# Kernel tuning notes

Hardware: AMD Instinct MI355X
Metric: run time of the kernel (lower is better)

Reference implementation:

```python
import jax, jax.numpy as jnp
import numpy as np

N_NODES = 100000
N_EDGES = 1600000
N_GRAPHS = 1024
D_NODE = 128
D_EDGE = 32
H1 = 64
H2 = 16


def _p(key, shape):
    return jax.random.normal(key, shape, dtype=jnp.float32) * 0.05


def setup_inputs() -> dict:
    key = jax.random.key(0)
    ks = jax.random.split(key, 24)
    x = jax.random.normal(ks[0], (N_NODES, D_NODE), dtype=jnp.float32)
    edge_index = jax.random.randint(ks[1], (2, N_EDGES), 0, N_NODES, dtype=jnp.int64)
    edge_attr = jax.random.normal(ks[2], (N_EDGES, D_EDGE), dtype=jnp.float32)
    batch = jnp.sort(jax.random.randint(ks[3], (N_NODES,), 0, N_GRAPHS, dtype=jnp.int64))
    # layer 1 (TransformerConv in=128, out=64, edge_dim=32, heads=1)
    Wq1, bq1 = _p(ks[4], (D_NODE, H1)), _p(ks[5], (H1,))
    Wk1, bk1 = _p(ks[6], (D_NODE, H1)), _p(ks[7], (H1,))
    Wv1, bv1 = _p(ks[8], (D_NODE, H1)), _p(ks[9], (H1,))
    We1 = _p(ks[10], (D_EDGE, H1))  # lin_edge has no bias in PyG
    Ws1, bs1 = _p(ks[11], (D_NODE, H1)), _p(ks[12], (H1,))  # skip / root weight
    # layer 2 (in=64, out=16)
    Wq2, bq2 = _p(ks[13], (H1, H2)), _p(ks[14], (H2,))
    Wk2, bk2 = _p(ks[15], (H1, H2)), _p(ks[16], (H2,))
    Wv2, bv2 = _p(ks[17], (H1, H2)), _p(ks[18], (H2,))
    We2 = _p(ks[19], (D_EDGE, H2))
    Ws2, bs2 = _p(ks[20], (H1, H2)), _p(ks[21], (H2,))
    # final fc
    Wf, bf = _p(ks[22], (H2, 1)), _p(ks[23], (1,))
    return dict(x=x, edge_attr=edge_attr,
                Wq1=Wq1, bq1=bq1, Wk1=Wk1, bk1=bk1, Wv1=Wv1, bv1=bv1, We1=We1, Ws1=Ws1, bs1=bs1,
                Wq2=Wq2, bq2=bq2, Wk2=Wk2, bk2=bk2, Wv2=Wv2, bv2=bv2, We2=We2, Ws2=Ws2, bs2=bs2,
                Wf=Wf, bf=bf, edge_index=edge_index, batch=batch)


def transformer_conv(x, edge_index, edge_attr, Wq, bq, Wk, bk, Wv, bv, We, Ws, bs):
    # PyG TransformerConv, heads=1, concat=True, root_weight=True
    n = x.shape[0]
    c = Wq.shape[1]
    src, dst = edge_index[0], edge_index[1]
    q = x @ Wq + bq                      # [N, C]
    k = x @ Wk + bk                      # [N, C]
    v = x @ Wv + bv                      # [N, C]
    e = edge_attr @ We                   # [E, C]
    ke = k[src] + e                      # [E, C]
    ve = v[src] + e                      # [E, C]
    score = jnp.sum(q[dst] * ke, axis=-1) / jnp.sqrt(jnp.float32(c))  # [E]
    # segment softmax over incoming edges of each dst node
    m = jax.ops.segment_max(score, dst, num_segments=n)
    a = jnp.exp(score - m[dst])
    den = jax.ops.segment_sum(a, dst, num_segments=n)
    alpha = a / (den[dst] + 1e-16)
    out = jax.ops.segment_sum(ve * alpha[:, None], dst, num_segments=n)  # [N, C]
    return out + x @ Ws + bs


def reference(x, edge_attr, Wq1, bq1, Wk1, bk1, Wv1, bv1, We1, Ws1, bs1,
              Wq2, bq2, Wk2, bk2, Wv2, bv2, We2, Ws2, bs2, Wf, bf,
              edge_index, batch):
    h = jax.nn.relu(transformer_conv(x, edge_index, edge_attr,
                                     Wq1, bq1, Wk1, bk1, Wv1, bv1, We1, Ws1, bs1))
    h = jax.nn.relu(transformer_conv(h, edge_index, edge_attr,
                                     Wq2, bq2, Wk2, bk2, Wv2, bv2, We2, Ws2, bs2))
    # global mean pool over graphs
    sums = jax.ops.segment_sum(h, batch, num_segments=N_GRAPHS)          # [G, 16]
    cnt = jax.ops.segment_sum(jnp.ones((h.shape[0],), h.dtype), batch, num_segments=N_GRAPHS)
    z = sums / jnp.maximum(cnt, 1.0)[:, None]
    return jax.nn.sigmoid(z @ Wf + bf)                                    # [G, 1]
```

## Files before the change

kernel.cpp:

```cpp
#include <hip/hip_runtime.h>
#include <hip/hip_bf16.h>
#include <math.h>

#define N_NODES 100000
#define N_EDGES 1600000
#define N_GRAPHS 1024
#define NB_SCAN ((N_NODES + 255) / 256)
#define NODES_PER_CHUNK 25000
#define CHUNK_EDGE_CAP 450000

static __device__ __forceinline__ float bf2f(ushort u) {
    return __uint_as_float(((unsigned)u) << 16);
}
static __device__ __forceinline__ ushort f2bf(float f) {
    unsigned x = __float_as_uint(f);
    return (ushort)((x + 0x7fffu + ((x >> 16) & 1u)) >> 16);
}

__global__ __launch_bounds__(256) void node_lin1(const float* __restrict__ x,
                          const float* __restrict__ Wq, const float* __restrict__ bq,
                          const float* __restrict__ Wk, const float* __restrict__ bk,
                          const float* __restrict__ Wv, const float* __restrict__ bv,
                          const float* __restrict__ Ws, const float* __restrict__ bs,
                          float* __restrict__ q, uint* __restrict__ kvt,
                          float* __restrict__ s) {
    __shared__ float xs[16][128];
    int tid = threadIdx.x;
    int nb = blockIdx.x * 16;
    for (int i = tid; i < 16 * 128; i += 256) xs[i >> 7][i & 127] = x[(size_t)nb * 128 + i];
    __syncthreads();
    int w = tid >> 6, t = tid & 63;
    const float* W = (w == 0) ? Wq : (w == 1) ? Wk : (w == 2) ? Wv : Ws;
    const float* b = (w == 0) ? bq : (w == 1) ? bk : (w == 2) ? bv : bs;
    float acc[16];
#pragma unroll
    for (int n = 0; n < 16; ++n) acc[n] = 0.f;
#pragma unroll 2
    for (int j = 0; j < 128; j += 4) {
        float w0 = W[j * 64 + t];
        float w1 = W[(j + 1) * 64 + t];
        float w2 = W[(j + 2) * 64 + t];
        float w3 = W[(j + 3) * 64 + t];
#pragma unroll
        for (int n = 0; n < 16; ++n) {
            float4 xv = *(const float4*)&xs[n][j];
            acc[n] += xv.x * w0 + xv.y * w1 + xv.z * w2 + xv.w * w3;
        }
    }
    float bb = b[t];
#pragma unroll
    for (int n = 0; n < 16; ++n) {
        int nn = nb + n;
        if (nn >= N_NODES) break;
        float r = acc[n] + bb;
        if (w == 0)      q[(size_t)nn * 64 + t] = r;
        else if (w == 1) ((ushort*)kvt)[((size_t)nn * 64 + t) * 2]     = f2bf(r);
        else if (w == 2) ((ushort*)kvt)[((size_t)nn * 64 + t) * 2 + 1] = f2bf(r);
        else             s[(size_t)nn * 64 + t] = r;
    }
}

__global__ __launch_bounds__(256) void node_lin2(const float* __restrict__ h,
                          const float* __restrict__ Wq, const float* __restrict__ bq,
                          const float* __restrict__ Wk, const float* __restrict__ bk,
                          const float* __restrict__ Wv, const float* __restrict__ bv,
                          const float* __restrict__ Ws, const float* __restrict__ bs,
                          float* __restrict__ q, uint* __restrict__ kvt,
                          float* __restrict__ s) {
    __shared__ float hs[32][65];
    int tid = threadIdx.x;
    int nb = blockIdx.x * 32;
    for (int i = tid; i < 32 * 64; i += 256) {
        int nn = nb + (i >> 6);
        hs[i >> 6][i & 63] = (nn < N_NODES) ? h[(size_t)nb * 64 + i] : 0.f;
    }
    __syncthreads();
    int w = tid >> 6, t = tid & 63, g = t >> 4, c = t & 15;
    const float* W = (w == 0) ? Wq : (w == 1) ? Wk : (w == 2) ? Wv : Ws;
    const float* b = (w == 0) ? bq : (w == 1) ? bk : (w == 2) ? bv : bs;
    float acc[8];
#pragma unroll
    for (int n = 0; n < 8; ++n) acc[n] = 0.f;
#pragma unroll 4
    for (int j = 0; j < 64; ++j) {
        float wv = W[j * 16 + c];
#pragma unroll
        for (int n = 0; n < 8; ++n) acc[n] += hs[g * 8 + n][j] * wv;
    }
    float bb = b[c];
#pragma unroll
    for (int n = 0; n < 8; ++n) {
        int nn = nb + g * 8 + n;
        if (nn >= N_NODES) break;
        float r = acc[n] + bb;
        if (w == 0)      q[(size_t)nn * 16 + c] = r;
        else if (w == 1) ((ushort*)kvt)[((size_t)nn * 16 + c) * 2]     = f2bf(r);
        else if (w == 2) ((ushort*)kvt)[((size_t)nn * 16 + c) * 2 + 1] = f2bf(r);
        else             s[(size_t)nn * 16 + c] = r;
    }
}

__global__ void hist_kernel(const int* __restrict__ ei, int* __restrict__ deg) {
    int e = blockIdx.x * blockDim.x + threadIdx.x;
    if (e < N_EDGES) atomicAdd(deg + ei[N_EDGES + e], 1);
}

__global__ __launch_bounds__(256) void scan_block(const int* __restrict__ deg,
        int* __restrict__ rowptr, int* __restrict__ bsum) {
    __shared__ int sd[256];
    int i = blockIdx.x * 256 + threadIdx.x;
    int v = (i < N_NODES) ? deg[i] : 0;
    sd[threadIdx.x] = v;
    __syncthreads();
    for (int off = 1; off < 256; off <<= 1) {
        int add = (threadIdx.x >= off) ? sd[threadIdx.x - off] : 0;
        __syncthreads();
        sd[threadIdx.x] += add;
        __syncthreads();
    }
    if (i < N_NODES) rowptr[i] = sd[threadIdx.x] - v;
    if (threadIdx.x == 255) bsum[blockIdx.x] = sd[255];
}

__global__ __launch_bounds__(512) void scan_bsum(int* __restrict__ bsum) {
    __shared__ int sd[512];
    int t = threadIdx.x;
    int v = (t < NB_SCAN) ? bsum[t] : 0;
    sd[t] = v;
    __syncthreads();
    for (int off = 1; off < 512; off <<= 1) {
        int add = (t >= off) ? sd[t - off] : 0;
        __syncthreads();
        sd[t] += add;
        __syncthreads();
    }
    if (t < NB_SCAN) bsum[t] = sd[t] - v;
}

__global__ void scan_add(int* __restrict__ rowptr, int* __restrict__ cursor,
                         const int* __restrict__ bsum) {
    int i = blockIdx.x * blockDim.x + threadIdx.x;
    if (i < N_NODES) {
        int r = rowptr[i] + bsum[i >> 8];
        rowptr[i] = r;
        cursor[i] = r;
    }
    if (i == 0) rowptr[N_NODES] = N_EDGES;
}

__global__ void scatter_kernel(const int* __restrict__ ei, int* __restrict__ cursor,
                               int2* __restrict__ sorted) {
    int e = blockIdx.x * blockDim.x + threadIdx.x;
    if (e >= N_EDGES) return;
    int d = ei[N_EDGES + e];
    int pos = atomicAdd(cursor + d, 1);
    sorted[pos] = make_int2(ei[e], e);
}

__global__ __launch_bounds__(256) void edge_mlp1(const int2* __restrict__ sorted,
        const int* __restrict__ rowptr, int n0, int n1,
        const float* __restrict__ ea, const float* __restrict__ We1,
        const float* __restrict__ We2,
        ushort* __restrict__ ep1, ushort* __restrict__ ep2) {
    __shared__ float ea_s[64][36];
    int pbeg = rowptr[n0], pend = rowptr[n1];
    int base = pbeg + blockIdx.x * 64;
    if (base >= pend) return;
    int nedges = pend - base; if (nedges > 64) nedges = 64;
    int tid = threadIdx.x;
    int e4 = tid >> 2, r = tid & 3;
    if (e4 < nedges) {
        int eid = sorted[base + e4].y;
        const float4* src = (const float4*)(ea + (size_t)eid * 32);
        ((float4*)ea_s[e4])[r * 2]     = src[r * 2];
        ((float4*)ea_s[e4])[r * 2 + 1] = src[r * 2 + 1];
    }
    __syncthreads();
    int w = tid >> 6, t = tid & 63;
    int c2 = t & 15, j0 = (t >> 4) * 8;
    float we[32];
#pragma unroll
    for (int j = 0; j < 32; ++j) we[j] = We1[j * 64 + t];
    float we2p[8];
#pragma unroll
    for (int i = 0; i < 8; ++i) we2p[i] = We2[(j0 + i) * 16 + c2];
    int e0 = w * 16;
    int ecnt = nedges - e0; if (ecnt > 16) ecnt = 16;
    for (int e = 0; e < ecnt; ++e) {
        const float4* row = (const float4*)ea_s[e0 + e];
        float et = 0.f;
#pragma unroll
        for (int r2 = 0; r2 < 8; ++r2) {
            float4 f = row[r2];
            et += f.x * we[4*r2] + f.y * we[4*r2+1] + f.z * we[4*r2+2] + f.w * we[4*r2+3];
        }
        ep1[(size_t)(base - pbeg + e0 + e) * 64 + t] = f2bf(et);
        const float* rowf = ea_s[e0 + e] + j0;
        float p2 = rowf[0] * we2p[0] + rowf[1] * we2p[1] + rowf[2] * we2p[2]
                 + rowf[3] * we2p[3] + rowf[4] * we2p[4] + rowf[5] * we2p[5]
                 + rowf[6] * we2p[6] + rowf[7] * we2p[7];
        p2 += __shfl_xor(p2, 16, 64);
        p2 += __shfl_xor(p2, 32, 64);
        if (t < 16) ep2[(size_t)(base + e0 + e) * 16 + t] = f2bf(p2);
    }
}

__global__ __launch_bounds__(256) void agg_l1(const int2* __restrict__ sorted,
        const int* __restrict__ rowptr, const ushort* __restrict__ ep1,
        const float* __restrict__ q, const uint* __restrict__ kvt,
        float* __restrict__ h, int n0, int n1) {
    int w = threadIdx.x >> 6, t = threadIdx.x & 63;
    int n = n0 + blockIdx.x * 4 + w;
    if (n >= n1) return;
    int g = t >> 4, c = t & 15;
    int pbeg = rowptr[n0];
    float4 q4 = ((const float4*)(q + (size_t)n * 64))[c];
    int beg = rowptr[n], end = rowptr[n + 1];
    float den = 0.f;
    float ax = 0.f, ay = 0.f, az = 0.f, aw = 0.f;
    int idx = beg + g;
    for (; idx + 4 < end; idx += 8) {
        int sA = sorted[idx].x, sB = sorted[idx + 4].x;
        uint4 kvA = ((const uint4*)(kvt + (size_t)sA * 64))[c];
        uint4 kvB = ((const uint4*)(kvt + (size_t)sB * 64))[c];
        ushort4 eA = ((const ushort4*)(ep1 + (size_t)(idx - pbeg) * 64))[c];
        ushort4 eB = ((const ushort4*)(ep1 + (size_t)(idx + 4 - pbeg) * 64))[c];
        float eA0 = bf2f(eA.x), eA1 = bf2f(eA.y), eA2 = bf2f(eA.z), eA3 = bf2f(eA.w);
        float eB0 = bf2f(eB.x), eB1 = bf2f(eB.y), eB2 = bf2f(eB.z), eB3 = bf2f(eB.w);
        float kA0 = bf2f((ushort)kvA.x), vA0 = bf2f((ushort)(kvA.x >> 16));
        float kA1 = bf2f((ushort)kvA.y), vA1 = bf2f((ushort)(kvA.y >> 16));
        float kA2 = bf2f((ushort)kvA.z), vA2 = bf2f((ushort)(kvA.z >> 16));
        float kA3 = bf2f((ushort)kvA.w), vA3 = bf2f((ushort)(kvA.w >> 16));
        float kB0 = bf2f((ushort)kvB.x), vB0 = bf2f((ushort)(kvB.x >> 16));
        float kB1 = bf2f((ushort)kvB.y), vB1 = bf2f((ushort)(kvB.y >> 16));
        float kB2 = bf2f((ushort)kvB.z), vB2 = bf2f((ushort)(kvB.z >> 16));
        float kB3 = bf2f((ushort)kvB.w), vB3 = bf2f((ushort)(kvB.w >> 16));
        float pA = q4.x * (kA0 + eA0) + q4.y * (kA1 + eA1)
                 + q4.z * (kA2 + eA2) + q4.w * (kA3 + eA3);
        float pB = q4.x * (kB0 + eB0) + q4.y * (kB1 + eB1)
                 + q4.z * (kB2 + eB2) + q4.w * (kB3 + eB3);
        pA += __shfl_xor(pA, 1, 64); pB += __shfl_xor(pB, 1, 64);
        pA += __shfl_xor(pA, 2, 64); pB += __shfl_xor(pB, 2, 64);
        pA += __shfl_xor(pA, 4, 64); pB += __shfl_xor(pB, 4, 64);
        pA += __shfl_xor(pA, 8, 64); pB += __shfl_xor(pB, 8, 64);
        float aA = __expf(pA * 0.125f), aB = __expf(pB * 0.125f);
        den += aA + aB;
        ax += aA * (vA0 + eA0) + aB * (vB0 + eB0);
        ay += aA * (vA1 + eA1) + aB * (vB1 + eB1);
        az += aA * (vA2 + eA2) + aB * (vB2 + eB2);
        aw += aA * (vA3 + eA3) + aB * (vB3 + eB3);
    }
    if (idx < end) {
        int s = sorted[idx].x;
        uint4 kv4 = ((const uint4*)(kvt + (size_t)s * 64))[c];
        ushort4 e4 = ((const ushort4*)(ep1 + (size_t)(idx - pbeg) * 64))[c];
        float e0 = bf2f(e4.x), e1 = bf2f(e4.y), e2 = bf2f(e4.z), e3 = bf2f(e4.w);
        float k0 = bf2f((ushort)kv4.x), v0 = bf2f((ushort)(kv4.x >> 16));
        float k1 = bf2f((ushort)kv4.y), v1 = bf2f((ushort)(kv4.y >> 16));
        float k2 = bf2f((ushort)kv4.z), v2 = bf2f((ushort)(kv4.z >> 16));
        float k3 = bf2f((ushort)kv4.w), v3 = bf2f((ushort)(kv4.w >> 16));
        float p = q4.x * (k0 + e0) + q4.y * (k1 + e1) + q4.z * (k2 + e2) + q4.w * (k3 + e3);
        p += __shfl_xor(p, 1, 64);
        p += __shfl_xor(p, 2, 64);
        p += __shfl_xor(p, 4, 64);
        p += __shfl_xor(p, 8, 64);
        float a = __expf(p * 0.125f);
        den += a;
        ax += a * (v0 + e0); ay += a * (v1 + e1);
        az += a * (v2 + e2); aw += a * (v3 + e3);
    }
    den += __shfl_xor(den, 16, 64); den += __shfl_xor(den, 32, 64);
    ax += __shfl_xor(ax, 16, 64);   ax += __shfl_xor(ax, 32, 64);
    ay += __shfl_xor(ay, 16, 64);   ay += __shfl_xor(ay, 32, 64);
    az += __shfl_xor(az, 16, 64);   az += __shfl_xor(az, 32, 64);
    aw += __shfl_xor(aw, 16, 64);   aw += __shfl_xor(aw, 32, 64);
    if (g == 0) {
        float4* hp = (float4*)(h + (size_t)n * 64) + c;
        float4 hv = *hp;
        float d = den + 1e-16f;
        float4 o;
        o.x = ax / d + hv.x; o.x = o.x > 0.f ? o.x : 0.f;
        o.y = ay / d + hv.y; o.y = o.y > 0.f ? o.y : 0.f;
        o.z = az / d + hv.z; o.z = o.z > 0.f ? o.z : 0.f;
        o.w = aw / d + hv.w; o.w = o.w > 0.f ? o.w : 0.f;
        *hp = o;
    }
}

__global__ __launch_bounds__(256) void agg_l2(const int2* __restrict__ sorted,
        const int* __restrict__ rowptr, const ushort* __restrict__ ep2,
        const float* __restrict__ q, const uint* __restrict__ kvt,
        const float* __restrict__ skip, const int* __restrict__ batch,
        float* __restrict__ sums, float* __restrict__ cnt) {
    int w = threadIdx.x >> 6, t = threadIdx.x & 63;
    int n = blockIdx.x * 4 + w;
    if (n >= N_NODES) return;
    int g = t >> 4, c = t & 15;
    float qv = q[(size_t)n * 16 + c];
    int beg = rowptr[n], end = rowptr[n + 1];
    float den = 0.f, acc = 0.f;
    int idx = beg + g;
    for (; idx + 12 < end; idx += 16) {
        int sA = sorted[idx].x,      sB = sorted[idx + 4].x;
        int sC = sorted[idx + 8].x,  sD = sorted[idx + 12].x;
        uint kvA = kvt[(size_t)sA * 16 + c];
        uint kvB = kvt[(size_t)sB * 16 + c];
        uint kvC = kvt[(size_t)sC * 16 + c];
        uint kvD = kvt[(size_t)sD * 16 + c];
        float eA = bf2f(ep2[(size_t)idx * 16 + c]);
        float eB = bf2f(ep2[(size_t)(idx + 4) * 16 + c]);
        float eC = bf2f(ep2[(size_t)(idx + 8) * 16 + c]);
        float eD = bf2f(ep2[(size_t)(idx + 12) * 16 + c]);
        float pA = qv * (bf2f((ushort)kvA) + eA);
        float pB = qv * (bf2f((ushort)kvB) + eB);
        float pC = qv * (bf2f((ushort)kvC) + eC);
        float pD = qv * (bf2f((ushort)kvD) + eD);
        pA += __shfl_xor(pA, 8, 64); pB += __shfl_xor(pB, 8, 64);
        pC += __shfl_xor(pC, 8, 64); pD += __shfl_xor(pD, 8, 64);
        pA += __shfl_xor(pA, 4, 64); pB += __shfl_xor(pB, 4, 64);
        pC += __shfl_xor(pC, 4, 64); pD += __shfl_xor(pD, 4, 64);
        pA += __shfl_xor(pA, 2, 64); pB += __shfl_xor(pB, 2, 64);
        pC += __shfl_xor(pC, 2, 64); pD += __shfl_xor(pD, 2, 64);
        pA += __shfl_xor(pA, 1, 64); pB += __shfl_xor(pB, 1, 64);
        pC += __shfl_xor(pC, 1, 64); pD += __shfl_xor(pD, 1, 64);
        float aA = __expf(pA * 0.25f), aB = __expf(pB * 0.25f);
        float aC = __expf(pC * 0.25f), aD = __expf(pD * 0.25f);
        den += (aA + aB) + (aC + aD);
        acc += aA * (bf2f((ushort)(kvA >> 16)) + eA)
             + aB * (bf2f((ushort)(kvB >> 16)) + eB)
             + aC * (bf2f((ushort)(kvC >> 16)) + eC)
             + aD * (bf2f((ushort)(kvD >> 16)) + eD);
    }
    for (; idx + 4 < end; idx += 8) {
        int sA = sorted[idx].x, sB = sorted[idx + 4].x;
        uint kvA = kvt[(size_t)sA * 16 + c];
        uint kvB = kvt[(size_t)sB * 16 + c];
        float eA = bf2f(ep2[(size_t)idx * 16 + c]);
        float eB = bf2f(ep2[(size_t)(idx + 4) * 16 + c]);
        float pA = qv * (bf2f((ushort)kvA) + eA);
        float pB = qv * (bf2f((ushort)kvB) + eB);
        pA += __shfl_xor(pA, 8, 64); pB += __shfl_xor(pB, 8, 64);
        pA += __shfl_xor(pA, 4, 64); pB += __shfl_xor(pB, 4, 64);
        pA += __shfl_xor(pA, 2, 64); pB += __shfl_xor(pB, 2, 64);
        pA += __shfl_xor(pA, 1, 64); pB += __shfl_xor(pB, 1, 64);
        float aA = __expf(pA * 0.25f), aB = __expf(pB * 0.25f);
        den += aA + aB;
        acc += aA * (bf2f((ushort)(kvA >> 16)) + eA)
             + aB * (bf2f((ushort)(kvB >> 16)) + eB);
    }
    if (idx < end) {
        int s = sorted[idx].x;
        uint kvp = kvt[(size_t)s * 16 + c];
        float e2 = bf2f(ep2[(size_t)idx * 16 + c]);
        float p = qv * (bf2f((ushort)kvp) + e2);
        p += __shfl_xor(p, 8, 64);
        p += __shfl_xor(p, 4, 64);
        p += __shfl_xor(p, 2, 64);
        p += __shfl_xor(p, 1, 64);
        float a = __expf(p * 0.25f);
        den += a;
        acc += a * (bf2f((ushort)(kvp >> 16)) + e2);
    }
    den += __shfl_xor(den, 16, 64);
    den += __shfl_xor(den, 32, 64);
    acc += __shfl_xor(acc, 16, 64);
    acc += __shfl_xor(acc, 32, 64);
    if (t < 16) {
        float r2 = acc / (den + 1e-16f) + skip[(size_t)n * 16 + c];
        r2 = r2 > 0.f ? r2 : 0.f;
        int gb = batch[n];
        atomicAdd(sums + gb * 16 + c, r2);
        if (c == 0) atomicAdd(cnt + gb, 1.0f);
    }
}

__global__ void final_fc(const float* __restrict__ sums, const float* __restrict__ cnt,
                         const float* __restrict__ Wf, const float* __restrict__ bf,
                         float* __restrict__ out) {
    int g = blockIdx.x * blockDim.x + threadIdx.x;
    if (g >= N_GRAPHS) return;
    float cc = cnt[g];
    cc = cc > 1.f ? cc : 1.f;
    float acc = bf[0];
#pragma unroll
    for (int c = 0; c < 16; ++c) acc += (sums[g * 16 + c] / cc) * Wf[c];
    out[g] = 1.f / (1.f + expf(-acc));
}

extern "C" void kernel_launch(void* const* d_in, const int* in_sizes, int n_in,
                              void* d_out, int out_size, void* d_ws, size_t ws_size,
                              hipStream_t stream) {
    const float* x    = (const float*)d_in[0];
    const float* ea   = (const float*)d_in[1];
    const float* Wq1  = (const float*)d_in[2];
    const float* bq1  = (const float*)d_in[3];
    const float* Wk1  = (const float*)d_in[4];
    const float* bk1  = (const float*)d_in[5];
    const float* Wv1  = (const float*)d_in[6];
    const float* bv1  = (const float*)d_in[7];
    const float* We1  = (const float*)d_in[8];
    const float* Ws1  = (const float*)d_in[9];
    const float* bs1  = (const float*)d_in[10];
    const float* Wq2  = (const float*)d_in[11];
    const float* bq2  = (const float*)d_in[12];
    const float* Wk2  = (const float*)d_in[13];
    const float* bk2  = (const float*)d_in[14];
    const float* Wv2  = (const float*)d_in[15];
    const float* bv2  = (const float*)d_in[16];
    const float* We2  = (const float*)d_in[17];
    const float* Ws2  = (const float*)d_in[18];
    const float* bs2  = (const float*)d_in[19];
    const float* Wf   = (const float*)d_in[20];
    const float* bf   = (const float*)d_in[21];
    const int*   ei   = (const int*)d_in[22];
    const int*   batch= (const int*)d_in[23];
    float* out = (float*)d_out;

    float* ws = (float*)d_ws;
    size_t off = 0;
    float* q1    = ws + off;          off += (size_t)N_NODES * 64;
    uint* kvt1   = (uint*)(ws + off); off += (size_t)N_NODES * 64;
    float* s1    = ws + off;          off += (size_t)N_NODES * 64;
    float* q2    = ws + off;          off += (size_t)N_NODES * 16;
    uint* kvt2   = (uint*)(ws + off); off += (size_t)N_NODES * 16;
    float* s2    = ws + off;          off += (size_t)N_NODES * 16;
    int2* sorted = (int2*)(ws + off); off += (size_t)N_EDGES * 2;
    ushort* ep1  = (ushort*)(ws + off); off += (size_t)CHUNK_EDGE_CAP * 32;
    ushort* ep2  = (ushort*)(ws + off); off += (size_t)N_EDGES * 8;
    int* rowptr  = (int*)(ws + off);  off += N_NODES + 2;
    int* cursor  = (int*)(ws + off);  off += N_NODES;
    int* bsum    = (int*)(ws + off);  off += 512;
    float* zerop = ws + off;
    int*   deg   = (int*)(ws + off);  off += N_NODES;
    float* sums  = ws + off;          off += (size_t)N_GRAPHS * 16;
    float* cnt   = ws + off;          off += N_GRAPHS;
    size_t zero_bytes = ((size_t)N_NODES + N_GRAPHS * 16 + N_GRAPHS) * sizeof(float);
    hipMemsetAsync(zerop, 0, zero_bytes, stream);

    hist_kernel<<<(N_EDGES + 255) / 256, 256, 0, stream>>>(ei, deg);
    scan_block<<<NB_SCAN, 256, 0, stream>>>(deg, rowptr, bsum);
    scan_bsum<<<1, 512, 0, stream>>>(bsum);
    scan_add<<<NB_SCAN, 256, 0, stream>>>(rowptr, cursor, bsum);
    scatter_kernel<<<(N_EDGES + 255) / 256, 256, 0, stream>>>(ei, cursor, sorted);

    node_lin1<<<(N_NODES + 15) / 16, 256, 0, stream>>>(x, Wq1, bq1, Wk1, bk1, Wv1, bv1,
                                                       Ws1, bs1, q1, kvt1, s1);
    int mlp_blocks = (CHUNK_EDGE_CAP + 63) / 64;
    for (int c = 0; c < 4; ++c) {
        int n0 = c * NODES_PER_CHUNK;
        int n1 = (c + 1) * NODES_PER_CHUNK;
        if (n1 > N_NODES) n1 = N_NODES;
        edge_mlp1<<<mlp_blocks, 256, 0, stream>>>(sorted, rowptr, n0, n1, ea,
                                                  We1, We2, ep1, ep2);
        agg_l1<<<(NODES_PER_CHUNK + 3) / 4, 256, 0, stream>>>(sorted, rowptr, ep1,
                                                              q1, kvt1, s1, n0, n1);
    }

    node_lin2<<<(N_NODES + 31) / 32, 256, 0, stream>>>(s1, Wq2, bq2, Wk2, bk2, Wv2, bv2,
                                                       Ws2, bs2, q2, kvt2, s2);
    agg_l2<<<(N_NODES + 3) / 4, 256, 0, stream>>>(sorted, rowptr, ep2, q2, kvt2,
                                                  s2, batch, sums, cnt);

    final_fc<<<(N_GRAPHS + 255) / 256, 256, 0, stream>>>(sums, cnt, Wf, bf, out);
}
```

Before: 862.7 us.

## Compute layer-1 node projections with fp16 MFMA instead of scalar FMA

Converts x to fp16 and prepacks the four layer-1 weight matrices into MFMA fragment layout, then computes q/k/v/skip projections with 16x16x32 f16 MFMA instructions, 64 nodes per block. This replaces the scalar FP32 FMA loop in node_lin1 and is meant to cut its compute time. The trade-off is two extra conversion kernels, an extra pass over x, and reduced precision from fp16 inputs. The xh buffer reuses ep1 scratch space before the edge MLP writes to it.

```diff
diff --git a/kernel.cpp b/kernel.cpp
--- a/kernel.cpp
+++ b/kernel.cpp
@@ -1,5 +1,6 @@
 #include <hip/hip_runtime.h>
 #include <hip/hip_bf16.h>
+#include <hip/hip_fp16.h>
 #include <math.h>
 
 #define N_NODES 100000
@@ -9,6 +10,9 @@
 #define NODES_PER_CHUNK 25000
 #define CHUNK_EDGE_CAP 450000
 
+typedef _Float16 f16x8 __attribute__((ext_vector_type(8)));
+typedef float f32x4 __attribute__((ext_vector_type(4)));
+
 static __device__ __forceinline__ float bf2f(ushort u) {
     return __uint_as_float(((unsigned)u) << 16);
 }
@@ -17,46 +21,101 @@
     return (ushort)((x + 0x7fffu + ((x >> 16) & 1u)) >> 16);
 }
 
-__global__ __launch_bounds__(256) void node_lin1(const float* __restrict__ x,
-                          const float* __restrict__ Wq, const float* __restrict__ bq,
-                          const float* __restrict__ Wk, const float* __restrict__ bk,
-                          const float* __restrict__ Wv, const float* __restrict__ bv,
-                          const float* __restrict__ Ws, const float* __restrict__ bs,
-                          float* __restrict__ q, uint* __restrict__ kvt,
-                          float* __restrict__ s) {
-    __shared__ float xs[16][128];
+__global__ __launch_bounds__(256) void conv_x(const float* __restrict__ x,
+                                              __half* __restrict__ xh) {
+    int i = blockIdx.x * blockDim.x + threadIdx.x;
+    const float4* src = (const float4*)x;
+    float4 a = src[2 * i], b = src[2 * i + 1];
+    __half2 h0 = __floats2half2_rn(a.x, a.y);
+    __half2 h1 = __floats2half2_rn(a.z, a.w);
+    __half2 h2 = __floats2half2_rn(b.x, b.y);
+    __half2 h3 = __floats2half2_rn(b.z, b.w);
+    uint4 o = make_uint4(*(uint*)&h0, *(uint*)&h1, *(uint*)&h2, *(uint*)&h3);
+    ((uint4*)xh)[i] = o;
+}
+
+__global__ __launch_bounds__(256) void prepack_W(const float* __restrict__ Wq,
+        const float* __restrict__ Wk, const float* __restrict__ Wv,
+        const float* __restrict__ Ws, __half* __restrict__ Bpack) {
+    int tid = blockIdx.x * 256 + threadIdx.x;
+    if (tid >= 4 * 4 * 4 * 64) return;
+    int lane = tid & 63, nt = (tid >> 6) & 3, kt = (tid >> 8) & 3, w = (tid >> 10) & 3;
+    const float* W = (w == 0) ? Wq : (w == 1) ? Wk : (w == 2) ? Wv : Ws;
+    int col = nt * 16 + (lane & 15);
+    int kbase = kt * 32 + (lane >> 4) * 8;
+    __half* dst = Bpack + (size_t)tid * 8;
+#pragma unroll
+    for (int j = 0; j < 8; ++j) dst[j] = __float2half(W[(kbase + j) * 64 + col]);
+}
+
+__global__ __launch_bounds__(256) void node_lin1_mfma(const __half* __restrict__ xh,
+        const float* __restrict__ bq, const float* __restrict__ bk,
+        const float* __restrict__ bv, const float* __restrict__ bs,
+        const __half* __restrict__ Bpack,
+        float* __restrict__ q, uint* __restrict__ kvt, float* __restrict__ s) {
+    __shared__ _Float16 As[64][136];
     int tid = threadIdx.x;
-    int nb = blockIdx.x * 16;
-    for (int i = tid; i < 16 * 128; i += 256) xs[i >> 7][i & 127] = x[(size_t)nb * 128 + i];
+    int nb = blockIdx.x * 64;
+    {
+        int row = tid >> 2, seg = tid & 3;
+        int nn = nb + row;
+        uint4* dst = (uint4*)&As[row][seg * 32];
+        if (nn < N_NODES) {
+            const uint4* sp = (const uint4*)(xh + (size_t)nn * 128 + seg * 32);
+            dst[0] = sp[0]; dst[1] = sp[1]; dst[2] = sp[2]; dst[3] = sp[3];
+        } else {
+            uint4 z = make_uint4(0, 0, 0, 0);
+            dst[0] = z; dst[1] = z; dst[2] = z; dst[3] = z;
+        }
+    }
     __syncthreads();
-    int w = tid >> 6, t = tid & 63;
-    const float* W = (w == 0) ? Wq : (w == 1) ? Wk : (w == 2) ? Wv : Ws;
-    const float* b = (w == 0) ? bq : (w == 1) ? bk : (w == 2) ? bv : bs;
-    float acc[16];
-#pragma unroll
-    for (int n = 0; n < 16; ++n) acc[n] = 0.f;
-#pragma unroll 2
-    for (int j = 0; j < 128; j += 4) {
-        float w0 = W[j * 64 + t];
-        float w1 = W[(j + 1) * 64 + t];
-        float w2 = W[(j + 2) * 64 + t];
-        float w3 = W[(j + 3) * 64 + t];
-#pragma unroll
-        for (int n = 0; n < 16; ++n) {
-            float4 xv = *(const float4*)&xs[n][j];
-            acc[n] += xv.x * w0 + xv.y * w1 + xv.z * w2 + xv.w * w3;
+    int wv = tid >> 6, lane = tid & 63;
+    const f16x8* Bp = (const f16x8*)Bpack;
+    f16x8 Bf[4][4];
+#pragma unroll
+    for (int kt = 0; kt < 4; ++kt)
+#pragma unroll
+        for (int nt = 0; nt < 4; ++nt)
+            Bf[kt][nt] = Bp[((wv * 4 + kt) * 4 + nt) * 64 + lane];
+    f32x4 acc[4][4];
+#pragma unroll
+    for (int mt = 0; mt < 4; ++mt)
+#pragma unroll
+        for (int nt = 0; nt < 4; ++nt) acc[mt][nt] = (f32x4){0.f, 0.f, 0.f, 0.f};
+    int arow = lane & 15, akoff = (lane >> 4) * 8;
+#pragma unroll
+    for (int kt = 0; kt < 4; ++kt) {
+        f16x8 a[4];
+#pragma unroll
+        for (int mt = 0; mt < 4; ++mt)
+            a[mt] = *(const f16x8*)&As[mt * 16 + arow][kt * 32 + akoff];
+#pragma unroll
+        for (int mt = 0; mt < 4; ++mt)
+#pragma unroll
+            for (int nt = 0; nt < 4; ++nt)
+                acc[mt][nt] = __builtin_amdgcn_mfma_f32_16x16x32_f16(
+                    a[mt], Bf[kt][nt], acc[mt][nt], 0, 0, 0);
+    }
+    const float* bvec = (wv == 0) ? bq : (wv == 1) ? bk : (wv == 2) ? bv : bs;
+    int colw = lane & 15;
+    int rgrp = (lane >> 4) * 4;
+#pragma unroll
+    for (int nt = 0; nt < 4; ++nt) {
+        float bias = bvec[nt * 16 + colw];
+        int col = nt * 16 + colw;
+#pragma unroll
+        for (int mt = 0; mt < 4; ++mt) {
+#pragma unroll
+            for (int r = 0; r < 4; ++r) {
+                int node = nb + mt * 16 + rgrp + r;
+                if (node >= N_NODES) continue;
+                float val = acc[mt][nt][r] + bias;
+                if (wv == 0)      q[(size_t)node * 64 + col] = val;
+                else if (wv == 1) ((ushort*)kvt)[((size_t)node * 64 + col) * 2]     = f2bf(val);
+                else if (wv == 2) ((ushort*)kvt)[((size_t)node * 64 + col) * 2 + 1] = f2bf(val);
+                else              s[(size_t)node * 64 + col] = val;
+            }
         }
-    }
-    float bb = b[t];
-#pragma unroll
-    for (int n = 0; n < 16; ++n) {
-        int nn = nb + n;
-        if (nn >= N_NODES) break;
-        float r = acc[n] + bb;
-        if (w == 0)      q[(size_t)nn * 64 + t] = r;
-        else if (w == 1) ((ushort*)kvt)[((size_t)nn * 64 + t) * 2]     = f2bf(r);
-        else if (w == 2) ((ushort*)kvt)[((size_t)nn * 64 + t) * 2 + 1] = f2bf(r);
-        else             s[(size_t)nn * 64 + t] = r;
     }
 }
 
@@ -435,7 +494,14 @@
     float* sums  = ws + off;          off += (size_t)N_GRAPHS * 16;
     float* cnt   = ws + off;          off += N_GRAPHS;
     size_t zero_bytes = ((size_t)N_NODES + N_GRAPHS * 16 + N_GRAPHS) * sizeof(float);
+    off = (off + 3) & ~(size_t)3;
+    __half* Bpack = (__half*)(ws + off); off += 16384;
+    __half* xh = (__half*)ep1;
+
     hipMemsetAsync(zerop, 0, zero_bytes, stream);
+
+    conv_x<<<6250, 256, 0, stream>>>(x, xh);
+    prepack_W<<<16, 256, 0, stream>>>(Wq1, Wk1, Wv1, Ws1, Bpack);
 
     hist_kernel<<<(N_EDGES + 255) / 256, 256, 0, stream>>>(ei, deg);
     scan_block<<<NB_SCAN, 256, 0, stream>>>(deg, rowptr, bsum);
@@ -443,8 +509,9 @@
     scan_add<<<NB_SCAN, 256, 0, stream>>>(rowptr, cursor, bsum);
     scatter_kernel<<<(N_EDGES + 255) / 256, 256, 0, stream>>>(ei, cursor, sorted);
 
-    node_lin1<<<(N_NODES + 15) / 16, 256, 0, stream>>>(x, Wq1, bq1, Wk1, bk1, Wv1, bv1,
-                                                       Ws1, bs1, q1, kvt1, s1);
+    node_lin1_mfma<<<(N_NODES + 63) / 64, 256, 0, stream>>>(xh, bq1, bk1, bv1, bs1,
+                                                            Bpack, q1, kvt1, s1);
+
     int mlp_blocks = (CHUNK_EDGE_CAP + 63) / 64;
     for (int c = 0; c < 4; ++c) {
         int n0 = c * NODES_PER_CHUNK;
```

Measured after the change: 782.3 us (median of 3 runs). 9.3% less time.
